# Kernel tuning notes

Measured on AMD Instinct MI355X. Metric: run time of the kernel, lower is better.

Reference implementation:

```python
import jax, jax.numpy as jnp
import numpy as np

B, T, N, D, L = 32, 12, 1024, 64, 2


def setup_inputs() -> dict:
    key = jax.random.key(0)
    ks = jax.random.split(key, 8)
    s = 1.0 / np.sqrt(D)
    p = lambda k, shape: jax.random.normal(k, shape, jnp.float32) * s
    return {
        "x": jax.random.normal(ks[0], (B, T, N, D), jnp.float32),
        "Wq_x": p(ks[1], (L, D, D)),
        "Wk_x": p(ks[2], (L, D, D)),
        "Wq_h": p(ks[3], (L, D, D)),
        "Wk_h": p(ks[4], (L, D, D)),
        "Wx": p(ks[5], (L, D, 3 * D)),
        "Wh": p(ks[6], (L, D, 3 * D)),
        "b": jnp.zeros((L, 3 * D), jnp.float32),
    }


def _attend(z, Wq, Wk):
    # z: [B,N,D] -> node-to-node graph attention
    q = z @ Wq
    k = z @ Wk
    scores = jnp.einsum('bnd,bmd->bnm', q, k) / jnp.sqrt(jnp.asarray(z.shape[-1], z.dtype))
    a = jax.nn.softmax(scores, axis=-1)          # [B,N,N]
    return a, jnp.einsum('bnm,bmd->bnd', a, z)   # attended features


def reference(x, Wq_x, Wk_x, Wq_h, Wk_h, Wx, Wh, b):
    Bv, Tv, Nv, Dv = x.shape
    Lv = Wx.shape[0]
    h0 = jnp.zeros((Bv, Lv, Nv, Dv), x.dtype)
    a0 = jnp.zeros((Bv, Lv, Nv, Nv), x.dtype)

    def step(carry, x_t):
        hidden, _, _ = carry  # only last-step attn is kept (matches torch: attn_i/attn_h overwritten each tick)
        out = x_t
        hs, axs, ahs = [], [], []
        for l in range(Lv):  # small fixed layer loop
            a_x, gx = _attend(out, Wq_x[l], Wk_x[l])
            a_h, gh = _attend(hidden[:, l], Wq_h[l], Wk_h[l])
            gates = gx @ Wx[l] + b[l]   # [B,N,3D]
            hg = gh @ Wh[l]
            iz, ir, inn = jnp.split(gates, 3, axis=-1)
            hz, hr, hn = jnp.split(hg, 3, axis=-1)
            zg = jax.nn.sigmoid(iz + hz)
            rg = jax.nn.sigmoid(ir + hr)
            ng = jnp.tanh(inn + rg * hn)
            h_new = (1.0 - zg) * ng + zg * hidden[:, l]
            hs.append(h_new)
            axs.append(a_x)
            ahs.append(a_h)
            out = h_new
        new_carry = (jnp.stack(hs, 1), jnp.stack(axs, 1), jnp.stack(ahs, 1))
        return new_carry, out

    (hidden, attn_x, attn_h), outs = jax.lax.scan(step, (h0, a0, a0), jnp.swapaxes(x, 0, 1))
    output = jnp.swapaxes(outs, 0, 1)  # [B,T,N,D]
    return output, hidden, attn_x, attn_h
```

## Files before the change

### kernel.cpp

```cpp
#include <hip/hip_runtime.h>
#include <math.h>

#define B_ 32
#define T_ 12
#define N_ 1024
#define D_ 64
#define L_ 2

constexpr int ND  = N_ * D_;
constexpr int BND = B_ * N_ * D_;
constexpr long long NN = (long long)N_ * N_;

__global__ __launch_bounds__(256) void qk_kernel(
    const float* __restrict__ zx, int zx_sb,
    const float* __restrict__ zh, int zh_sb,
    const float* __restrict__ Wqx, const float* __restrict__ Wkx,
    const float* __restrict__ Wqh, const float* __restrict__ Wkh,
    float* __restrict__ qx, float* __restrict__ kx,
    float* __restrict__ qh, float* __restrict__ kh)
{
    int i0 = blockIdx.x * 128;
    int b  = blockIdx.y;
    int which = blockIdx.z;
    const float* z; const float* W; float* out;
    if (which == 0)      { z = zx + (size_t)b * zx_sb; W = Wqx; out = qx; }
    else if (which == 1) { z = zx + (size_t)b * zx_sb; W = Wkx; out = kx; }
    else if (which == 2) { z = zh + (size_t)b * zh_sb; W = Wqh; out = qh; }
    else                 { z = zh + (size_t)b * zh_sb; W = Wkh; out = kh; }
    out += (size_t)b * ND;

    __shared__ float4 Zs[128 * 16];
    __shared__ float  Ws[16][64][4];

    int tid = threadIdx.x;
    #pragma unroll
    for (int it = 0; it < 8; ++it) {
        int idx = tid + it * 256;
        int r = idx >> 4, c = idx & 15;
        Zs[r * 16 + (c ^ (r & 15))] =
            *(const float4*)(z + (size_t)(i0 + r) * 64 + c * 4);
    }
    #pragma unroll
    for (int it = 0; it < 4; ++it) {
        int idx = tid + it * 256;
        int kk = idx >> 4, n4 = (idx & 15) * 4;
        float4 v = *(const float4*)(W + (size_t)kk * 64 + n4);
        Ws[kk >> 2][n4 + 0][kk & 3] = v.x;
        Ws[kk >> 2][n4 + 1][kk & 3] = v.y;
        Ws[kk >> 2][n4 + 2][kk & 3] = v.z;
        Ws[kk >> 2][n4 + 3][kk & 3] = v.w;
    }
    __syncthreads();

    int tx = tid & 15, ty = tid >> 4;
    float acc[8][4];
    #pragma unroll
    for (int i = 0; i < 8; ++i)
        #pragma unroll
        for (int j = 0; j < 4; ++j) acc[i][j] = 0.f;

    #pragma unroll 2
    for (int s = 0; s < 16; ++s) {
        float4 af[8], wf[4];
        #pragma unroll
        for (int h = 0; h < 2; ++h)
            #pragma unroll
            for (int ii = 0; ii < 4; ++ii) {
                int m = h * 64 + ty * 4 + ii;
                af[h * 4 + ii] = Zs[m * 16 + (s ^ (m & 15))];
            }
        #pragma unroll
        for (int j = 0; j < 4; ++j)
            wf[j] = *(const float4*)&Ws[s][tx + 16 * j][0];
        #pragma unroll
        for (int i = 0; i < 8; ++i)
            #pragma unroll
            for (int j = 0; j < 4; ++j) {
                acc[i][j] += af[i].x * wf[j].x;
                acc[i][j] += af[i].y * wf[j].y;
                acc[i][j] += af[i].z * wf[j].z;
                acc[i][j] += af[i].w * wf[j].w;
            }
    }
    #pragma unroll
    for (int i = 0; i < 8; ++i) {
        int m = (i >> 2) * 64 + ty * 4 + (i & 3);
        #pragma unroll
        for (int j = 0; j < 4; ++j)
            out[(size_t)(i0 + m) * 64 + tx + 16 * j] = acc[i][j];
    }
}

__global__ __launch_bounds__(256) void scores_kernel(
    const float* __restrict__ qx, const float* __restrict__ kx,
    const float* __restrict__ qh, const float* __restrict__ kh,
    float* __restrict__ ax, float* __restrict__ ah, int l)
{
    int i0 = blockIdx.x * 128, j0 = blockIdx.y * 128;
    int att = blockIdx.z & 1, b = blockIdx.z >> 1;
    const float* q = (att ? qh : qx) + (size_t)b * ND;
    const float* k = (att ? kh : kx) + (size_t)b * ND;
    float* S = (att ? ah : ax) + (size_t)(b * L_ + l) * NN;

    __shared__ float4 Qs[128 * 16];
    __shared__ float4 Ks[128 * 16];

    int tid = threadIdx.x;
    #pragma unroll
    for (int it = 0; it < 8; ++it) {
        int idx = tid + it * 256;
        int r = idx >> 4, c = idx & 15;
        int sw = c ^ (r & 15);
        Qs[r * 16 + sw] = *(const float4*)(q + (size_t)(i0 + r) * 64 + c * 4);
        Ks[r * 16 + sw] = *(const float4*)(k + (size_t)(j0 + r) * 64 + c * 4);
    }
    __syncthreads();

    int tx = tid & 15, ty = tid >> 4;
    float acc[8][8];
    #pragma unroll
    for (int i = 0; i < 8; ++i)
        #pragma unroll
        for (int j = 0; j < 8; ++j) acc[i][j] = 0.f;

    #pragma unroll 2
    for (int s = 0; s < 16; ++s) {
        float4 qf[8], kf[8];
        #pragma unroll
        for (int h = 0; h < 2; ++h)
            #pragma unroll
            for (int ii = 0; ii < 4; ++ii) {
                int m = h * 64 + ty * 4 + ii;
                qf[h * 4 + ii] = Qs[m * 16 + (s ^ (m & 15))];
            }
        #pragma unroll
        for (int j = 0; j < 8; ++j) {
            int n = tx + 16 * j;
            kf[j] = Ks[n * 16 + (s ^ (n & 15))];
        }
        #pragma unroll
        for (int i = 0; i < 8; ++i)
            #pragma unroll
            for (int j = 0; j < 8; ++j) {
                acc[i][j] += qf[i].x * kf[j].x;
                acc[i][j] += qf[i].y * kf[j].y;
                acc[i][j] += qf[i].z * kf[j].z;
                acc[i][j] += qf[i].w * kf[j].w;
            }
    }

    #pragma unroll
    for (int i = 0; i < 8; ++i) {
        int m = (i >> 2) * 64 + ty * 4 + (i & 3);
        float* Srow = S + (size_t)(i0 + m) * N_ + j0;
        #pragma unroll
        for (int j = 0; j < 8; ++j)
            Srow[tx + 16 * j] = acc[i][j] * 0.125f;
    }
}

__global__ __launch_bounds__(256) void softmax_kernel(
    float* __restrict__ ax, float* __restrict__ ah, int l)
{
    int i = blockIdx.x, b = blockIdx.y, att = blockIdx.z;
    float* row = (att ? ah : ax) + (size_t)(b * L_ + l) * NN + (size_t)i * N_;
    int tid = threadIdx.x;

    float4 v = ((const float4*)row)[tid];
    float m = fmaxf(fmaxf(v.x, v.y), fmaxf(v.z, v.w));
    #pragma unroll
    for (int off = 32; off; off >>= 1)
        m = fmaxf(m, __shfl_xor(m, off, 64));

    __shared__ float red_m[4], red_s[4];
    if ((tid & 63) == 0) red_m[tid >> 6] = m;
    __syncthreads();
    m = fmaxf(fmaxf(red_m[0], red_m[1]), fmaxf(red_m[2], red_m[3]));

    float e0 = __expf(v.x - m), e1 = __expf(v.y - m);
    float e2 = __expf(v.z - m), e3 = __expf(v.w - m);
    float s = e0 + e1 + e2 + e3;
    #pragma unroll
    for (int off = 32; off; off >>= 1)
        s += __shfl_xor(s, off, 64);
    if ((tid & 63) == 0) red_s[tid >> 6] = s;
    __syncthreads();
    s = red_s[0] + red_s[1] + red_s[2] + red_s[3];

    float inv = 1.f / s;
    ((float4*)row)[tid] = make_float4(e0 * inv, e1 * inv, e2 * inv, e3 * inv);
}

__global__ __launch_bounds__(256) void av_kernel(
    const float* __restrict__ ax, const float* __restrict__ ah,
    const float* __restrict__ zx, int zx_sb,
    const float* __restrict__ zh, int zh_sb,
    float* __restrict__ gx, float* __restrict__ gh, int l)
{
    int i0 = blockIdx.x * 128;
    int att = blockIdx.y & 1, b = blockIdx.y >> 1;
    const float* a = (att ? ah : ax) + (size_t)(b * L_ + l) * NN;
    const float* z = att ? (zh + (size_t)b * zh_sb) : (zx + (size_t)b * zx_sb);
    float* out = (att ? gh : gx) + (size_t)b * ND;

    __shared__ float4 As[128 * 16];
    __shared__ float  Zs[16][64][4];

    int tid = threadIdx.x;
    int tx = tid & 15, ty = tid >> 4;
    float acc[8][4];
    #pragma unroll
    for (int i = 0; i < 8; ++i)
        #pragma unroll
        for (int j = 0; j < 4; ++j) acc[i][j] = 0.f;

    for (int kc = 0; kc < 16; ++kc) {
        __syncthreads();
        #pragma unroll
        for (int it = 0; it < 8; ++it) {
            int idx = tid + it * 256;
            int r = idx >> 4, c = idx & 15;
            As[r * 16 + (c ^ (r & 15))] =
                *(const float4*)(a + (size_t)(i0 + r) * N_ + kc * 64 + c * 4);
        }
        #pragma unroll
        for (int it = 0; it < 4; ++it) {
            int idx = tid + it * 256;
            int kk = idx >> 4, n4 = (idx & 15) * 4;
            float4 v = *(const float4*)(z + (size_t)(kc * 64 + kk) * 64 + n4);
            Zs[kk >> 2][n4 + 0][kk & 3] = v.x;
            Zs[kk >> 2][n4 + 1][kk & 3] = v.y;
            Zs[kk >> 2][n4 + 2][kk & 3] = v.z;
            Zs[kk >> 2][n4 + 3][kk & 3] = v.w;
        }
        __syncthreads();

        #pragma unroll 2
        for (int s = 0; s < 16; ++s) {
            float4 af[8], zf[4];
            #pragma unroll
            for (int h = 0; h < 2; ++h)
                #pragma unroll
                for (int ii = 0; ii < 4; ++ii) {
                    int m = h * 64 + ty * 4 + ii;
                    af[h * 4 + ii] = As[m * 16 + (s ^ (m & 15))];
                }
            #pragma unroll
            for (int j = 0; j < 4; ++j)
                zf[j] = *(const float4*)&Zs[s][tx + 16 * j][0];
            #pragma unroll
            for (int i = 0; i < 8; ++i)
                #pragma unroll
                for (int j = 0; j < 4; ++j) {
                    acc[i][j] += af[i].x * zf[j].x;
                    acc[i][j] += af[i].y * zf[j].y;
                    acc[i][j] += af[i].z * zf[j].z;
                    acc[i][j] += af[i].w * zf[j].w;
                }
        }
    }

    #pragma unroll
    for (int i = 0; i < 8; ++i) {
        int m = (i >> 2) * 64 + ty * 4 + (i & 3);
        #pragma unroll
        for (int j = 0; j < 4; ++j)
            out[(size_t)(i0 + m) * 64 + tx + 16 * j] = acc[i][j];
    }
}

__global__ __launch_bounds__(256) void gru_kernel(
    const float* __restrict__ gx, const float* __restrict__ gh,
    const float* __restrict__ Wxl, const float* __restrict__ Whl,
    const float* __restrict__ bl,
    float* __restrict__ hid, float* __restrict__ y, int l, int t)
{
    int n0 = blockIdx.x * 32;
    int b  = blockIdx.y;
    const float* gxb = gx + (size_t)b * ND;
    const float* ghb = gh + (size_t)b * ND;

    __shared__ float Gx[32][65], Gh[32][65];
    int tid = threadIdx.x;
    #pragma unroll
    for (int i = 0; i < 8; ++i) {
        int idx = tid + i * 256;
        int r = idx >> 6, c = idx & 63;
        Gx[r][c] = gxb[(size_t)(n0 + r) * 64 + c];
        Gh[r][c] = ghb[(size_t)(n0 + r) * 64 + c];
    }
    __syncthreads();

    int d  = tid & 63;
    int rg = tid >> 6;
    float iz[8] = {0}, ir[8] = {0}, in_[8] = {0};
    float hz[8] = {0}, hr[8] = {0}, hn[8] = {0};

    #pragma unroll 2
    for (int k = 0; k < 64; ++k) {
        float wx0 = Wxl[k * 192 + d];
        float wx1 = Wxl[k * 192 + 64 + d];
        float wx2 = Wxl[k * 192 + 128 + d];
        float wh0 = Whl[k * 192 + d];
        float wh1 = Whl[k * 192 + 64 + d];
        float wh2 = Whl[k * 192 + 128 + d];
        #pragma unroll
        for (int r = 0; r < 8; ++r) {
            float a = Gx[rg * 8 + r][k];
            float h = Gh[rg * 8 + r][k];
            iz[r] += a * wx0; ir[r] += a * wx1; in_[r] += a * wx2;
            hz[r] += h * wh0; hr[r] += h * wh1; hn[r] += h * wh2;
        }
    }

    float b0 = bl[d], b1 = bl[64 + d], b2 = bl[128 + d];
    #pragma unroll
    for (int r = 0; r < 8; ++r) {
        int row = n0 + rg * 8 + r;
        size_t hidx = ((size_t)(b * L_ + l) * N_ + row) * 64 + d;
        float ho = hid[hidx];
        float zg  = 1.f / (1.f + __expf(-(iz[r] + b0 + hz[r])));
        float rg_ = 1.f / (1.f + __expf(-(ir[r] + b1 + hr[r])));
        float ng  = tanhf(in_[r] + b2 + rg_ * hn[r]);
        float hnew = (1.f - zg) * ng + zg * ho;
        hid[hidx] = hnew;
        if (y) y[((size_t)(b * T_ + t) * N_ + row) * 64 + d] = hnew;
    }
}

extern "C" void kernel_launch(void* const* d_in, const int* in_sizes, int n_in,
                              void* d_out, int out_size, void* d_ws, size_t ws_size,
                              hipStream_t stream)
{
    const float* x    = (const float*)d_in[0];
    const float* Wq_x = (const float*)d_in[1];
    const float* Wk_x = (const float*)d_in[2];
    const float* Wq_h = (const float*)d_in[3];
    const float* Wk_h = (const float*)d_in[4];
    const float* Wx   = (const float*)d_in[5];
    const float* Wh   = (const float*)d_in[6];
    const float* bias = (const float*)d_in[7];

    float* outp = (float*)d_out;
    float* y   = outp;
    float* hid = y + (size_t)B_ * T_ * N_ * D_;
    float* ax  = hid + (size_t)B_ * L_ * N_ * D_;
    float* ah  = ax + (size_t)B_ * L_ * NN;

    float* ws = (float*)d_ws;
    float* qx = ws;
    float* kx = qx + BND;
    float* qh = kx + BND;
    float* kh = qh + BND;
    float* gx = kh + BND;
    float* gh = gx + BND;

    hipMemsetAsync(hid, 0, sizeof(float) * (size_t)B_ * L_ * N_ * D_, stream);

    for (int t = 0; t < T_; ++t) {
        for (int l = 0; l < L_; ++l) {
            const float* zx; int zx_sb;
            if (l == 0) { zx = x + (size_t)t * ND; zx_sb = T_ * ND; }
            else        { zx = hid;                zx_sb = L_ * ND; }
            const float* zh = hid + (size_t)l * ND; int zh_sb = L_ * ND;

            qk_kernel<<<dim3(8, B_, 4), 256, 0, stream>>>(
                zx, zx_sb, zh, zh_sb,
                Wq_x + l * 4096, Wk_x + l * 4096,
                Wq_h + l * 4096, Wk_h + l * 4096,
                qx, kx, qh, kh);

            scores_kernel<<<dim3(8, 8, 2 * B_), 256, 0, stream>>>(
                qx, kx, qh, kh, ax, ah, l);

            softmax_kernel<<<dim3(N_, B_, 2), 256, 0, stream>>>(ax, ah, l);

            av_kernel<<<dim3(8, 2 * B_), 256, 0, stream>>>(
                ax, ah, zx, zx_sb, zh, zh_sb, gx, gh, l);

            gru_kernel<<<dim3(32, B_), 256, 0, stream>>>(
                gx, gh, Wx + l * D_ * 192, Wh + l * D_ * 192, bias + l * 192,
                hid, (l == L_ - 1) ? y : nullptr, l, t);
        }
    }
}
```

Before: 10.50 ms.

## Fuse scores, softmax and AV into flash-style attention for non-final timesteps

For all timesteps except the last, the separate scores, softmax and AV kernels are replaced by a transpose of V plus a fused online-softmax attention kernel. Only the final step's attention matrices are part of the output, so the intermediate N×N matrices no longer need to be written to and read back from global memory. The fused kernel double-buffers K/V tiles through registers and shared memory and uses XOR-swizzled layouts. Trade-offs are an extra transpose kernel, a large shared-memory footprint that caps occupancy at one 512-thread block per CU, and reuse of the attention output buffer as scratch.

```diff
diff --git a/kernel.cpp b/kernel.cpp
--- a/kernel.cpp
+++ b/kernel.cpp
@@ -88,6 +88,206 @@
         #pragma unroll
         for (int j = 0; j < 4; ++j)
             out[(size_t)(i0 + m) * 64 + tx + 16 * j] = acc[i][j];
+    }
+}
+
+__global__ __launch_bounds__(256) void transpose_v(
+    const float* __restrict__ zx, int zx_sb,
+    const float* __restrict__ zh, int zh_sb,
+    float* __restrict__ vxT, float* __restrict__ vhT)
+{
+    int n0 = blockIdx.x * 64;
+    int b  = blockIdx.y;
+    int w  = blockIdx.z;
+    const float* src = w ? (zh + (size_t)b * zh_sb) : (zx + (size_t)b * zx_sb);
+    float* dst = (w ? vhT : vxT) + (size_t)b * ND;
+
+    __shared__ float tile[64][65];
+    int tid = threadIdx.x;
+    #pragma unroll
+    for (int it = 0; it < 4; ++it) {
+        int idx = tid + it * 256;
+        int r = idx >> 4, c4 = (idx & 15) * 4;
+        float4 vv = *(const float4*)(src + (size_t)(n0 + r) * 64 + c4);
+        tile[r][c4] = vv.x; tile[r][c4 + 1] = vv.y;
+        tile[r][c4 + 2] = vv.z; tile[r][c4 + 3] = vv.w;
+    }
+    __syncthreads();
+    #pragma unroll
+    for (int it = 0; it < 4; ++it) {
+        int idx = tid + it * 256;
+        int d = idx >> 4, n4 = (idx & 15) * 4;
+        float4 vv = make_float4(tile[n4][d], tile[n4 + 1][d],
+                                tile[n4 + 2][d], tile[n4 + 3][d]);
+        *(float4*)(dst + (size_t)d * N_ + n0 + n4) = vv;
+    }
+}
+
+__global__ __launch_bounds__(512, 1) void fused_attn(
+    const float* __restrict__ qx, const float* __restrict__ kx,
+    const float* __restrict__ qh, const float* __restrict__ kh,
+    const float* __restrict__ vxT, const float* __restrict__ vhT,
+    float* __restrict__ gx, float* __restrict__ gh)
+{
+    int bid = blockIdx.y * 8 + blockIdx.x;
+    int xcd = bid & 7, seq = bid >> 3;
+    int yy = xcd + 8 * (seq >> 3);
+    int i0 = (seq & 7) * 128;
+    int att = yy & 1, b = yy >> 1;
+
+    const float* q  = (att ? qh  : qx ) + (size_t)b * ND;
+    const float* kk = (att ? kh  : kx ) + (size_t)b * ND;
+    const float* vT = (att ? vhT : vxT) + (size_t)b * ND;
+    float* out = (att ? gh : gx) + (size_t)b * ND;
+
+    __shared__ float4 Qs[128 * 16];
+    __shared__ float4 Ks[2][64 * 16];
+    __shared__ float4 Vs[2][64 * 16];
+    __shared__ float4 Ps[128 * 16];
+
+    int tid = threadIdx.x;
+    int tx = tid & 15, ty = tid >> 4;
+
+    #pragma unroll
+    for (int it = 0; it < 4; ++it) {
+        int idx = tid + it * 512;
+        int r = idx >> 4, c = idx & 15;
+        float4 vq = *(const float4*)(q + (size_t)(i0 + r) * 64 + c * 4);
+        vq.x *= 0.125f; vq.y *= 0.125f; vq.z *= 0.125f; vq.w *= 0.125f;
+        Qs[r * 16 + (c ^ (r & 15))] = vq;
+    }
+
+    float4 kst[2], vst[2];
+    #pragma unroll
+    for (int it = 0; it < 2; ++it) {
+        int idx = tid + it * 512;
+        int r = idx >> 4, c4 = (idx & 15) * 4;
+        kst[it] = *(const float4*)(kk + (size_t)r * 64 + c4);
+        vst[it] = *(const float4*)(vT + (size_t)r * N_ + c4);
+    }
+    #pragma unroll
+    for (int it = 0; it < 2; ++it) {
+        int idx = tid + it * 512;
+        int r = idx >> 4, c = idx & 15;
+        int sw = r * 16 + (c ^ (r & 15));
+        Ks[0][sw] = kst[it];
+        Vs[0][sw] = vst[it];
+    }
+    __syncthreads();
+
+    float acc[4][4] = {{0.f}};
+    float mrow[4], lrow[4];
+    #pragma unroll
+    for (int ii = 0; ii < 4; ++ii) { mrow[ii] = -1e30f; lrow[ii] = 0.f; }
+
+    for (int kc = 0; kc < 16; ++kc) {
+        int buf = kc & 1;
+        if (kc < 15) {
+            const float* kn = kk + (size_t)(kc + 1) * 64 * 64;
+            const float* vn = vT + (size_t)(kc + 1) * 64;
+            #pragma unroll
+            for (int it = 0; it < 2; ++it) {
+                int idx = tid + it * 512;
+                int r = idx >> 4, c4 = (idx & 15) * 4;
+                kst[it] = *(const float4*)(kn + (size_t)r * 64 + c4);
+                vst[it] = *(const float4*)(vn + (size_t)r * N_ + c4);
+            }
+        }
+        float sv[4][4] = {{0.f}};
+        #pragma unroll 4
+        for (int s = 0; s < 16; ++s) {
+            float4 qf[4], kf[4];
+            #pragma unroll
+            for (int ii = 0; ii < 4; ++ii) {
+                int m = ty * 4 + ii;
+                qf[ii] = Qs[m * 16 + (s ^ (m & 15))];
+            }
+            #pragma unroll
+            for (int j = 0; j < 4; ++j) {
+                int n = tx + 16 * j;
+                kf[j] = Ks[buf][n * 16 + (s ^ (n & 15))];
+            }
+            #pragma unroll
+            for (int ii = 0; ii < 4; ++ii)
+                #pragma unroll
+                for (int j = 0; j < 4; ++j)
+                    sv[ii][j] += qf[ii].x * kf[j].x + qf[ii].y * kf[j].y
+                               + qf[ii].z * kf[j].z + qf[ii].w * kf[j].w;
+        }
+        float p[4][4];
+        #pragma unroll
+        for (int ii = 0; ii < 4; ++ii) {
+            float tm = fmaxf(fmaxf(sv[ii][0], sv[ii][1]),
+                             fmaxf(sv[ii][2], sv[ii][3]));
+            #pragma unroll
+            for (int off = 8; off; off >>= 1)
+                tm = fmaxf(tm, __shfl_xor(tm, off, 64));
+            float mn = fmaxf(mrow[ii], tm);
+            float sc = __expf(mrow[ii] - mn);
+            mrow[ii] = mn;
+            float rs = 0.f;
+            #pragma unroll
+            for (int j = 0; j < 4; ++j) {
+                float e = __expf(sv[ii][j] - mn);
+                p[ii][j] = e; rs += e;
+            }
+            #pragma unroll
+            for (int off = 8; off; off >>= 1)
+                rs += __shfl_xor(rs, off, 64);
+            lrow[ii] = lrow[ii] * sc + rs;
+            acc[ii][0] *= sc; acc[ii][1] *= sc;
+            acc[ii][2] *= sc; acc[ii][3] *= sc;
+        }
+        __syncthreads();
+        #pragma unroll
+        for (int ii = 0; ii < 4; ++ii) {
+            int m = ty * 4 + ii;
+            float* prow = (float*)&Ps[m * 16];
+            #pragma unroll
+            for (int j = 0; j < 4; ++j) {
+                int kcol = tx + 16 * j;
+                prow[(((kcol >> 2) ^ (m & 15)) << 2) + (kcol & 3)] = p[ii][j];
+            }
+        }
+        if (kc < 15) {
+            #pragma unroll
+            for (int it = 0; it < 2; ++it) {
+                int idx = tid + it * 512;
+                int r = idx >> 4, c = idx & 15;
+                int sw = r * 16 + (c ^ (r & 15));
+                Ks[buf ^ 1][sw] = kst[it];
+                Vs[buf ^ 1][sw] = vst[it];
+            }
+        }
+        __syncthreads();
+        #pragma unroll 4
+        for (int s = 0; s < 16; ++s) {
+            float4 af[4], zf[4];
+            #pragma unroll
+            for (int ii = 0; ii < 4; ++ii) {
+                int m = ty * 4 + ii;
+                af[ii] = Ps[m * 16 + (s ^ (m & 15))];
+            }
+            #pragma unroll
+            for (int j = 0; j < 4; ++j) {
+                int n = tx + 16 * j;
+                zf[j] = Vs[buf][n * 16 + (s ^ (n & 15))];
+            }
+            #pragma unroll
+            for (int ii = 0; ii < 4; ++ii)
+                #pragma unroll
+                for (int j = 0; j < 4; ++j)
+                    acc[ii][j] += af[ii].x * zf[j].x + af[ii].y * zf[j].y
+                                + af[ii].z * zf[j].z + af[ii].w * zf[j].w;
+        }
+    }
+    #pragma unroll
+    for (int ii = 0; ii < 4; ++ii) {
+        float inv = 1.f / lrow[ii];
+        int m = ty * 4 + ii;
+        #pragma unroll
+        for (int j = 0; j < 4; ++j)
+            out[(size_t)(i0 + m) * 64 + tx + 16 * j] = acc[ii][j] * inv;
     }
 }
 
@@ -355,6 +555,9 @@
     float* gx = kh + BND;
     float* gh = gx + BND;
 
+    float* vxT = ax;
+    float* vhT = ax + BND;
+
     hipMemsetAsync(hid, 0, sizeof(float) * (size_t)B_ * L_ * N_ * D_, stream);
 
     for (int t = 0; t < T_; ++t) {
@@ -370,13 +573,18 @@
                 Wq_h + l * 4096, Wk_h + l * 4096,
                 qx, kx, qh, kh);
 
-            scores_kernel<<<dim3(8, 8, 2 * B_), 256, 0, stream>>>(
-                qx, kx, qh, kh, ax, ah, l);
-
-            softmax_kernel<<<dim3(N_, B_, 2), 256, 0, stream>>>(ax, ah, l);
-
-            av_kernel<<<dim3(8, 2 * B_), 256, 0, stream>>>(
-                ax, ah, zx, zx_sb, zh, zh_sb, gx, gh, l);
+            if (t < T_ - 1) {
+                transpose_v<<<dim3(16, B_, 2), 256, 0, stream>>>(
+                    zx, zx_sb, zh, zh_sb, vxT, vhT);
+                fused_attn<<<dim3(8, 2 * B_), 512, 0, stream>>>(
+                    qx, kx, qh, kh, vxT, vhT, gx, gh);
+            } else {
+                scores_kernel<<<dim3(8, 8, 2 * B_), 256, 0, stream>>>(
+                    qx, kx, qh, kh, ax, ah, l);
+                softmax_kernel<<<dim3(N_, B_, 2), 256, 0, stream>>>(ax, ah, l);
+                av_kernel<<<dim3(8, 2 * B_), 256, 0, stream>>>(
+                    ax, ah, zx, zx_sb, zh, zh_sb, gx, gh, l);
+            }
 
             gru_kernel<<<dim3(32, B_), 256, 0, stream>>>(
                 gx, gh, Wx + l * D_ * 192, Wh + l * D_ * 192, bias + l * 192,
```

After: 10.82 ms. +3.0%, slower.
